# Kernel tuning notes

Measured on AMD Instinct MI355X. Metric: run time of the kernel, lower is better.

The kernel has to match this reference:

```python
import jax, jax.numpy as jnp
import numpy as np

B, C, N, K = 4, 192, 8192, 16
C_OUT = 192


def _gather_nodes(xs, idx):
    # xs: [B, C, N], idx: [B, N, K] -> [B, C, N, K]
    return jax.vmap(lambda xb, ib: xb[:, ib])(xs, idx)


def setup_inputs() -> dict:
    key = jax.random.key(0)
    k1, k2, k3 = jax.random.split(key, 3)
    x = jax.random.normal(k1, (B, C, N, 1), dtype=jnp.float32)
    x_0 = jnp.zeros((B, C, N, 1), dtype=jnp.float32)  # unused by forward, kept for interface
    edge_index = jax.random.randint(k2, (2, B, N, K), 0, N, dtype=jnp.int32)
    # 1x1 Conv2d(2C -> C_OUT) weight flattened to [C_OUT, 2C]
    W = jax.random.normal(k3, (C_OUT, 2 * C), dtype=jnp.float32) / np.sqrt(2 * C)
    b = jnp.zeros((C_OUT,), dtype=jnp.float32)
    return {"x": x, "x_0": x_0, "edge_index": edge_index, "W": W, "b": b}


def reference(x, x_0, edge_index, W, b):
    xs = x[..., 0]                       # [B, C, N]
    x_i = _gather_nodes(xs, edge_index[1])   # centers  [B, C, N, K]
    x_j = _gather_nodes(xs, edge_index[0])   # neighbors [B, C, N, K]
    rel = jnp.max(x_j - x_i, axis=-1)        # max-relative [B, C, N]
    y = jnp.concatenate([xs, rel], axis=1)   # [B, 2C, N]
    out = jnp.einsum('oc,bcn->bon', W, y) + b[None, :, None]  # 1x1 conv
    out = jax.nn.relu(out)
    return out[..., None]                # [B, C_OUT, N, 1]
```

## Files before the change

kernel.cpp:

```cpp
#include <hip/hip_runtime.h>
#include <hip/hip_fp16.h>

#define B_    4
#define C_    192
#define N_    8192
#define K_    16
#define O_    192
#define TWOC_ 384
#define BN_   (B_ * N_)

typedef __attribute__((ext_vector_type(8))) _Float16 half8;
typedef __attribute__((ext_vector_type(4))) _Float16 half4v;
typedef __attribute__((ext_vector_type(4))) float floatx4;

static __device__ __forceinline__ half8 shflx8(half8 v, int m) {
    union { half8 h; int i[4]; } u;
    u.h = v;
#pragma unroll
    for (int q = 0; q < 4; q++) u.i[q] = __shfl_xor(u.i[q], m, 64);
    return u.h;
}
static __device__ __forceinline__ half4v shflx4(half4v v, int m) {
    union { half4v h; int i[2]; } u;
    u.h = v;
#pragma unroll
    for (int q = 0; q < 2; q++) u.i[q] = __shfl_xor(u.i[q], m, 64);
    return u.h;
}

__global__ __launch_bounds__(256) void k_convert_w(const float* __restrict__ W,
                                                   unsigned short* __restrict__ Wb) {
    int i = blockIdx.x * 256 + threadIdx.x;
    if (i < O_ * TWOC_) {
        union { _Float16 h; unsigned short s; } v;
        v.h = (_Float16)W[i];
        Wb[i] = v.s;
    }
}

__global__ __launch_bounds__(256) void k_transpose(const float* __restrict__ x,
                                                   unsigned short* __restrict__ xt) {
    __shared__ float tile[32][33];
    int bid  = blockIdx.x;
    int xcd  = bid & 7;
    int b    = xcd >> 1;
    int half = xcd & 1;
    int slot = bid >> 3;
    int ct   = slot >> 7;
    int nt   = half * 128 + (slot & 127);
    int c0 = ct * 32, n0 = nt * 32;
    int tid = threadIdx.x;

    int cc  = tid >> 3;
    int nn4 = (tid & 7) * 4;
    const float* xp = x + ((size_t)b * C_ + c0 + cc) * N_ + n0 + nn4;
    float4 v = *(const float4*)xp;
    tile[nn4 + 0][cc] = v.x;
    tile[nn4 + 1][cc] = v.y;
    tile[nn4 + 2][cc] = v.z;
    tile[nn4 + 3][cc] = v.w;
    __syncthreads();

#pragma unroll
    for (int i = 0; i < 2; i++) {
        int id  = i * 256 + tid;
        int row = id >> 4;
        int ch2 = id & 15;
        union { _Float16 h[2]; unsigned int u; } p;
        p.h[0] = (_Float16)tile[row][ch2 * 2];
        p.h[1] = (_Float16)tile[row][ch2 * 2 + 1];
        *(unsigned int*)(xt + ((size_t)b * N_ + n0 + row) * C_ + c0 + ch2 * 2) = p.u;
    }
}

__global__ __launch_bounds__(256) void k_gather(const unsigned short* __restrict__ xt,
                                                const int* __restrict__ eidx,
                                                unsigned short* __restrict__ rt) {
    int tid  = threadIdx.x;
    int lane = tid & 63;
    int w    = tid >> 6;
    int part = lane & 15;
    int kg   = lane >> 4;

    int bid  = blockIdx.x;
    int xcd  = bid & 7;
    int b    = xcd >> 1;
    int half = xcd & 1;
    int slot = bid >> 3;
    int widx = slot * 4 + w;
    int nbase = half * 4096 + widx * 4;

    const unsigned short* xb = xt + (size_t)b * N_ * C_;
    const int* e0 = eidx + ((size_t)b * N_ + nbase) * K_;
    const int* e1 = e0 + (size_t)BN_ * K_;

#pragma unroll
    for (int nn = 0; nn < 4; nn++) {
        int4 j4 = *(const int4*)(e0 + nn * K_ + kg * 4);
        int4 i4 = *(const int4*)(e1 + nn * K_ + kg * 4);
        half8  m0;
        half4v m1;
#pragma unroll
        for (int it = 0; it < 4; it++) {
            int jn  = (it == 0) ? j4.x : (it == 1) ? j4.y : (it == 2) ? j4.z : j4.w;
            int in_ = (it == 0) ? i4.x : (it == 1) ? i4.y : (it == 2) ? i4.z : i4.w;
            const unsigned short* pj = xb + (size_t)jn * C_;
            const unsigned short* pi = xb + (size_t)in_ * C_;
            half8  a0 = *(const half8*)(pj + part * 8);
            half4v a1 = *(const half4v*)(pj + 128 + part * 4);
            half8  b0 = *(const half8*)(pi + part * 8);
            half4v b1 = *(const half4v*)(pi + 128 + part * 4);
            half8  d0 = a0 - b0;
            half4v d1 = a1 - b1;
            if (it == 0) { m0 = d0; m1 = d1; }
            else {
                m0 = __builtin_elementwise_max(m0, d0);
                m1 = __builtin_elementwise_max(m1, d1);
            }
        }
        m0 = __builtin_elementwise_max(m0, shflx8(m0, 16));
        m1 = __builtin_elementwise_max(m1, shflx4(m1, 16));
        m0 = __builtin_elementwise_max(m0, shflx8(m0, 32));
        m1 = __builtin_elementwise_max(m1, shflx4(m1, 32));

        if (kg == 0) {
            unsigned short* ro = rt + ((size_t)b * N_ + nbase + nn) * C_;
            *(half8*)(ro + part * 8)        = m0;
            *(half4v*)(ro + 128 + part * 4) = m1;
        }
    }
}

__global__ __launch_bounds__(256) void k_conv(const unsigned short* __restrict__ xt,
                                              const unsigned short* __restrict__ rt,
                                              const unsigned short* __restrict__ Wb,
                                              const float* __restrict__ bias,
                                              float* __restrict__ out) {
    __shared__ __align__(16) unsigned short ytile[64 * TWOC_];
    char* yb = (char*)ytile;

    int bid  = blockIdx.x;
    int xcd  = bid & 7;
    int b    = xcd >> 1;
    int slot = bid >> 3;
    int n0   = ((xcd & 1) * 64 + slot) * 64;

    int tid  = threadIdx.x;
    int wave = tid >> 6;
    int lane = tid & 63;
    int m16  = lane & 15;
    int quad = lane >> 4;

    const unsigned short* xsrc = xt + ((size_t)b * N_ + n0) * C_;
    const unsigned short* rsrc = rt + ((size_t)b * N_ + n0) * C_;
#pragma unroll
    for (int i = 0; i < 6; i++) {
        int id = i * 256 + tid;
        int row = id / 24, chunk = id % 24;
        int sw = (row & 7) << 4;
        half8 vx = *(const half8*)(xsrc + (size_t)row * C_ + chunk * 8);
        half8 vr = *(const half8*)(rsrc + (size_t)row * C_ + chunk * 8);
        *(half8*)(yb + row * 768 + ((chunk * 16) ^ sw))       = vx;
        *(half8*)(yb + row * 768 + 384 + ((chunk * 16) ^ sw)) = vr;
    }
    __syncthreads();

    const unsigned short* wbase = Wb + (size_t)(wave * 48 + m16) * TWOC_ + quad * 8;

    floatx4 acc[3][4];
#pragma unroll
    for (int i = 0; i < 3; i++)
#pragma unroll
        for (int j = 0; j < 4; j++) acc[i][j] = (floatx4){0.f, 0.f, 0.f, 0.f};

#pragma unroll 2
    for (int kt = 0; kt < 12; kt++) {
        half8 wf[3], yf[4];
#pragma unroll
        for (int i = 0; i < 3; i++)
            wf[i] = *(const half8*)(wbase + (size_t)(i * 16) * TWOC_ + kt * 32);
#pragma unroll
        for (int j = 0; j < 4; j++) {
            int row = j * 16 + m16;
            yf[j] = *(const half8*)(yb + row * 768 + ((kt * 64 + quad * 16) ^ ((row & 7) << 4)));
        }
#pragma unroll
        for (int i = 0; i < 3; i++)
#pragma unroll
            for (int j = 0; j < 4; j++)
                acc[i][j] = __builtin_amdgcn_mfma_f32_16x16x32_f16(wf[i], yf[j], acc[i][j], 0, 0, 0);
    }

#pragma unroll
    for (int i = 0; i < 3; i++) {
#pragma unroll
        for (int r = 0; r < 4; r++) {
            int o = wave * 48 + i * 16 + quad * 4 + r;
            float bv = bias[o];
#pragma unroll
            for (int j = 0; j < 4; j++) {
                int n = n0 + j * 16 + m16;
                out[((size_t)b * O_ + o) * N_ + n] = fmaxf(acc[i][j][r] + bv, 0.f);
            }
        }
    }
}

extern "C" void kernel_launch(void* const* d_in, const int* in_sizes, int n_in,
                              void* d_out, int out_size, void* d_ws, size_t ws_size,
                              hipStream_t stream) {
    const float* x    = (const float*)d_in[0];
    const int*   eidx = (const int*)d_in[2];
    const float* W    = (const float*)d_in[3];
    const float* bias = (const float*)d_in[4];
    float*       out  = (float*)d_out;

    unsigned short* Wb = (unsigned short*)d_ws;
    unsigned short* xt = (unsigned short*)((char*)d_ws + 147456);
    unsigned short* rt = (unsigned short*)((char*)d_ws + 12730368);

    k_convert_w<<<dim3((O_ * TWOC_ + 255) / 256), dim3(256), 0, stream>>>(W, Wb);
    k_transpose<<<dim3(6144), dim3(256), 0, stream>>>(x, xt);
    k_gather<<<dim3(2048), dim3(256), 0, stream>>>(xt, eidx, rt);
    k_conv<<<dim3(512), dim3(256), 0, stream>>>(xt, rt, Wb, bias, out);
}
```

Measured before the change: 135.9 us.

## Gather from LDS-resident channel slices instead of random global row loads

The gather now works channel-major. Each block stages four channels of one batch (all N nodes, packed as fp16 pairs) into shared memory, then each thread handles one node and does the K random lookups from LDS. A channel-major fp16 copy of x is written alongside the transposed copy in a merged prep kernel, which also handles the weight conversion. The aim is to replace scattered 384-byte global row gathers with LDS lookups, at the cost of re-reading the edge indices once per channel slice (48 times) and using 64 KB of LDS per block. The output store is also made nontemporal.

```diff
diff --git a/kernel.cpp b/kernel.cpp
--- a/kernel.cpp
+++ b/kernel.cpp
@@ -11,37 +11,39 @@
 
 typedef __attribute__((ext_vector_type(8))) _Float16 half8;
 typedef __attribute__((ext_vector_type(4))) _Float16 half4v;
+typedef __attribute__((ext_vector_type(2))) _Float16 half2v;
 typedef __attribute__((ext_vector_type(4))) float floatx4;
-
-static __device__ __forceinline__ half8 shflx8(half8 v, int m) {
-    union { half8 h; int i[4]; } u;
-    u.h = v;
-#pragma unroll
-    for (int q = 0; q < 4; q++) u.i[q] = __shfl_xor(u.i[q], m, 64);
-    return u.h;
-}
-static __device__ __forceinline__ half4v shflx4(half4v v, int m) {
-    union { half4v h; int i[2]; } u;
-    u.h = v;
-#pragma unroll
-    for (int q = 0; q < 2; q++) u.i[q] = __shfl_xor(u.i[q], m, 64);
-    return u.h;
-}
-
-__global__ __launch_bounds__(256) void k_convert_w(const float* __restrict__ W,
-                                                   unsigned short* __restrict__ Wb) {
-    int i = blockIdx.x * 256 + threadIdx.x;
-    if (i < O_ * TWOC_) {
-        union { _Float16 h; unsigned short s; } v;
-        v.h = (_Float16)W[i];
-        Wb[i] = v.s;
-    }
-}
-
-__global__ __launch_bounds__(256) void k_transpose(const float* __restrict__ x,
-                                                   unsigned short* __restrict__ xt) {
+typedef __attribute__((ext_vector_type(4))) float fvec4;
+typedef __attribute__((ext_vector_type(4))) int   ivec4;
+typedef __attribute__((ext_vector_type(4))) unsigned int uvec4;
+typedef __attribute__((ext_vector_type(2))) unsigned int uvec2;
+
+__global__ __launch_bounds__(256) void k_prep(const float* __restrict__ x,
+                                              const float* __restrict__ W,
+                                              unsigned short* __restrict__ xt,
+                                              unsigned short* __restrict__ xc,
+                                              unsigned short* __restrict__ Wb) {
+    int bid = blockIdx.x;
+    int tid = threadIdx.x;
+
+    if (bid >= 6144) {
+        int base = ((bid - 6144) * 256 + tid) * 16;
+        union { unsigned short u[16]; uvec4 v[2]; } o;
+#pragma unroll
+        for (int q = 0; q < 16; q += 4) {
+            fvec4 f = __builtin_nontemporal_load((const fvec4*)(W + base + q));
+            union { _Float16 h; unsigned short s; } c;
+            c.h = (_Float16)f.x; o.u[q + 0] = c.s;
+            c.h = (_Float16)f.y; o.u[q + 1] = c.s;
+            c.h = (_Float16)f.z; o.u[q + 2] = c.s;
+            c.h = (_Float16)f.w; o.u[q + 3] = c.s;
+        }
+        *(uvec4*)(Wb + base)     = o.v[0];
+        *(uvec4*)(Wb + base + 8) = o.v[1];
+        return;
+    }
+
     __shared__ float tile[32][33];
-    int bid  = blockIdx.x;
     int xcd  = bid & 7;
     int b    = xcd >> 1;
     int half = xcd & 1;
@@ -49,12 +51,21 @@
     int ct   = slot >> 7;
     int nt   = half * 128 + (slot & 127);
     int c0 = ct * 32, n0 = nt * 32;
-    int tid = threadIdx.x;
 
     int cc  = tid >> 3;
     int nn4 = (tid & 7) * 4;
     const float* xp = x + ((size_t)b * C_ + c0 + cc) * N_ + n0 + nn4;
-    float4 v = *(const float4*)xp;
+    fvec4 v = __builtin_nontemporal_load((const fvec4*)xp);
+
+    {
+        union { _Float16 h[4]; uvec2 u; } pc;
+        pc.h[0] = (_Float16)v.x;
+        pc.h[1] = (_Float16)v.y;
+        pc.h[2] = (_Float16)v.z;
+        pc.h[3] = (_Float16)v.w;
+        *(uvec2*)(xc + ((size_t)b * C_ + c0 + cc) * N_ + n0 + nn4) = pc.u;
+    }
+
     tile[nn4 + 0][cc] = v.x;
     tile[nn4 + 1][cc] = v.y;
     tile[nn4 + 2][cc] = v.z;
@@ -73,61 +84,75 @@
     }
 }
 
-__global__ __launch_bounds__(256) void k_gather(const unsigned short* __restrict__ xt,
+__global__ __launch_bounds__(256) void k_gather(const unsigned short* __restrict__ xc,
                                                 const int* __restrict__ eidx,
                                                 unsigned short* __restrict__ rt) {
-    int tid  = threadIdx.x;
-    int lane = tid & 63;
-    int w    = tid >> 6;
-    int part = lane & 15;
-    int kg   = lane >> 4;
+    __shared__ unsigned int lds[2 * N_];
 
     int bid  = blockIdx.x;
     int xcd  = bid & 7;
     int b    = xcd >> 1;
-    int half = xcd & 1;
-    int slot = bid >> 3;
-    int widx = slot * 4 + w;
-    int nbase = half * 4096 + widx * 4;
-
-    const unsigned short* xb = xt + (size_t)b * N_ * C_;
-    const int* e0 = eidx + ((size_t)b * N_ + nbase) * K_;
+    int hq   = xcd & 1;
+    int rest = bid >> 3;
+    int s    = rest >> 1;
+    int qq   = rest & 1;
+    int nq   = hq * 2 + qq;
+    int c0   = s * 4;
+    int nbase = nq * 2048;
+    int tid  = threadIdx.x;
+
+#pragma unroll
+    for (int p = 0; p < 2; p++) {
+        const unsigned short* ra = xc + ((size_t)b * C_ + c0 + 2 * p) * N_;
+        const unsigned short* rb = ra + N_;
+#pragma unroll
+        for (int i = 0; i < 4; i++) {
+            int n0 = i * 2048 + tid * 8;
+            uvec4 A = *(const uvec4*)(ra + n0);
+            uvec4 Bv = *(const uvec4*)(rb + n0);
+#pragma unroll
+            for (int q = 0; q < 4; q++) {
+                unsigned a = A[q], bb = Bv[q];
+                unsigned lo = (a & 0xffffu) | (bb << 16);
+                unsigned hi = (a >> 16) | (bb & 0xffff0000u);
+                uvec2 w2 = {lo, hi};
+                *(uvec2*)&lds[p * N_ + n0 + q * 2] = w2;
+            }
+        }
+    }
+    __syncthreads();
+
+    const int* e0 = eidx + (size_t)b * N_ * K_;
     const int* e1 = e0 + (size_t)BN_ * K_;
-
-#pragma unroll
-    for (int nn = 0; nn < 4; nn++) {
-        int4 j4 = *(const int4*)(e0 + nn * K_ + kg * 4);
-        int4 i4 = *(const int4*)(e1 + nn * K_ + kg * 4);
-        half8  m0;
-        half4v m1;
-#pragma unroll
-        for (int it = 0; it < 4; it++) {
-            int jn  = (it == 0) ? j4.x : (it == 1) ? j4.y : (it == 2) ? j4.z : j4.w;
-            int in_ = (it == 0) ? i4.x : (it == 1) ? i4.y : (it == 2) ? i4.z : i4.w;
-            const unsigned short* pj = xb + (size_t)jn * C_;
-            const unsigned short* pi = xb + (size_t)in_ * C_;
-            half8  a0 = *(const half8*)(pj + part * 8);
-            half4v a1 = *(const half4v*)(pj + 128 + part * 4);
-            half8  b0 = *(const half8*)(pi + part * 8);
-            half4v b1 = *(const half4v*)(pi + 128 + part * 4);
-            half8  d0 = a0 - b0;
-            half4v d1 = a1 - b1;
-            if (it == 0) { m0 = d0; m1 = d1; }
-            else {
-                m0 = __builtin_elementwise_max(m0, d0);
-                m1 = __builtin_elementwise_max(m1, d1);
+    unsigned short* rto = rt + (size_t)b * N_ * C_ + c0;
+
+#pragma unroll 2
+    for (int i = 0; i < 8; i++) {
+        int n = nbase + i * 256 + tid;
+        ivec4 J[4], I[4];
+#pragma unroll
+        for (int kq = 0; kq < 4; kq++) {
+            J[kq] = *(const ivec4*)(e0 + (size_t)n * K_ + kq * 4);
+            I[kq] = *(const ivec4*)(e1 + (size_t)n * K_ + kq * 4);
+        }
+        half2v m0 = {(_Float16)-65504.f, (_Float16)-65504.f};
+        half2v m1 = m0;
+#pragma unroll
+        for (int kq = 0; kq < 4; kq++)
+#pragma unroll
+            for (int e = 0; e < 4; e++) {
+                int jn  = J[kq][e];
+                int in_ = I[kq][e];
+                union { unsigned u; half2v h; } j0, j1, i0, i1;
+                j0.u = lds[jn];        j1.u = lds[N_ + jn];
+                i0.u = lds[in_];       i1.u = lds[N_ + in_];
+                m0 = __builtin_elementwise_max(m0, j0.h - i0.h);
+                m1 = __builtin_elementwise_max(m1, j1.h - i1.h);
             }
-        }
-        m0 = __builtin_elementwise_max(m0, shflx8(m0, 16));
-        m1 = __builtin_elementwise_max(m1, shflx4(m1, 16));
-        m0 = __builtin_elementwise_max(m0, shflx8(m0, 32));
-        m1 = __builtin_elementwise_max(m1, shflx4(m1, 32));
-
-        if (kg == 0) {
-            unsigned short* ro = rt + ((size_t)b * N_ + nbase + nn) * C_;
-            *(half8*)(ro + part * 8)        = m0;
-            *(half4v*)(ro + 128 + part * 4) = m1;
-        }
+        union { half2v h; unsigned u; } o0, o1;
+        o0.h = m0; o1.h = m1;
+        uvec2 ov = {o0.u, o1.u};
+        *(uvec2*)(rto + (size_t)n * C_) = ov;
     }
 }
 
@@ -200,7 +225,8 @@
 #pragma unroll
             for (int j = 0; j < 4; j++) {
                 int n = n0 + j * 16 + m16;
-                out[((size_t)b * O_ + o) * N_ + n] = fmaxf(acc[i][j][r] + bv, 0.f);
+                __builtin_nontemporal_store(fmaxf(acc[i][j][r] + bv, 0.f),
+                                            &out[((size_t)b * O_ + o) * N_ + n]);
             }
         }
     }
@@ -217,10 +243,10 @@
 
     unsigned short* Wb = (unsigned short*)d_ws;
     unsigned short* xt = (unsigned short*)((char*)d_ws + 147456);
-    unsigned short* rt = (unsigned short*)((char*)d_ws + 12730368);
-
-    k_convert_w<<<dim3((O_ * TWOC_ + 255) / 256), dim3(256), 0, stream>>>(W, Wb);
-    k_transpose<<<dim3(6144), dim3(256), 0, stream>>>(x, xt);
-    k_gather<<<dim3(2048), dim3(256), 0, stream>>>(xt, eidx, rt);
+    unsigned short* xc = (unsigned short*)((char*)d_ws + 12730368);
+    unsigned short* rt = (unsigned short*)((char*)d_ws + 25313280);
+
+    k_prep<<<dim3(6162), dim3(256), 0, stream>>>(x, W, xt, xc, Wb);
+    k_gather<<<dim3(768), dim3(256), 0, stream>>>(xc, eidx, rt);
     k_conv<<<dim3(512), dim3(256), 0, stream>>>(xt, rt, Wb, bias, out);
 }
```

Measured after the change: 144.3 us. +6.1%, slower.
